# Performance work log

Hardware: AMD Instinct MI355X
Metric: run time of the kernel (lower is better)

## Reference

```python
import jax, jax.numpy as jnp
import numpy as np

B, N, D0 = 128, 128, 512   # batch, n_objects, obj_dim
H, KD, R = 32, 64, 16      # n_heads, key_dim, n_relations
D = D0 + 1                 # with temporal tag

def setup_inputs() -> dict:
    key = jax.random.key(0)
    k1, k2, k3, k4, k5 = jax.random.split(key, 5)
    s = 0.02
    return {
        'obj_seq': jax.random.normal(k1, (B, N, D0), jnp.float32),
        'W_k':  jax.random.normal(k2, (KD, D), jnp.float32) * s,
        'W_q1': jax.random.normal(k3, (H * KD, D * N), jnp.float32) * s,
        'W_q2': jax.random.normal(k4, (H * KD, D * N), jnp.float32) * s,
        'W_s':  jax.random.normal(k5, (R, D), jnp.float32) * s,
    }

def reference(obj_seq, W_k, W_q1, W_q2, W_s):
    b, n, _ = obj_seq.shape
    # append temporal tag channel: obj -> [B, N, D]
    tag = jnp.broadcast_to(jnp.arange(n, dtype=obj_seq.dtype)[None, :, None], (b, n, 1))
    obj = jnp.concatenate([obj_seq, tag], axis=2)
    flat = obj.reshape(b, -1)                      # [B, N*D]
    Q1 = (flat @ W_q1.T).reshape(b, H, KD)         # [B, H, KD]
    Q2 = (flat @ W_q2.T).reshape(b, H, KD)
    K = obj @ W_k.T                                # [B, N, KD]
    # scores [B, N, H], softmax over objects (dim=1 in torch)
    A1 = jax.nn.softmax(jnp.einsum('bhk,bnk->bnh', Q1, K), axis=1)
    A2 = jax.nn.softmax(jnp.einsum('bhk,bnk->bnh', Q2, K), axis=1)
    # attention-weighted object sums: [B, H, D]
    E1 = jnp.einsum('bnh,bnd->bhd', A1, obj)
    E2 = jnp.einsum('bnh,bnd->bhd', A2, obj)
    Dr = E1 @ W_s.T - E2 @ W_s.T                   # [B, H, R]
    Dr = jnp.concatenate([Dr, E1[:, :, -1:], E2[:, :, -1:]], axis=2)  # [B, H, R+2]
    return Dr.reshape(b, -1)                       # [B, H*(R+2)]
```

## Files before the change

### kernel.cpp

```cpp
#include <hip/hip_runtime.h>
#include <cstdint>

typedef _Float16 f16;
typedef _Float16 f16x8 __attribute__((ext_vector_type(8)));
typedef short s16x8 __attribute__((ext_vector_type(8)));
typedef unsigned u32x4 __attribute__((ext_vector_type(4)));
typedef float f32x4 __attribute__((ext_vector_type(4)));
typedef float floatx4 __attribute__((ext_vector_type(4)));

#define KTOT 65664
#define KSTEPS 2052
#define DP 544

__device__ __forceinline__ void gload_lds16(const void* g, void* l) {
  __builtin_amdgcn_global_load_lds(
      (const __attribute__((address_space(1))) void*)g,
      (__attribute__((address_space(3))) void*)l, 16, 0, 0);
}

__device__ __forceinline__ unsigned bfpack(float e0, float e1) {
  return (__float_as_uint(e0) >> 16) | (__float_as_uint(e1) & 0xffff0000u);
}
__device__ __forceinline__ float bfhi(float x) {
  return __uint_as_float(__float_as_uint(x) & 0xffff0000u);
}

__global__ void prep_flat(const float* __restrict__ obj_seq, char* __restrict__ flatA) {
  int o = blockIdx.x * 256 + threadIdx.x;
  int row = o & 127;
  int k8 = (o >> 7) & 3;
  int pl = (o >> 9) & 1;
  int kb = o >> 10;
  int k0 = kb * 32 + k8 * 8;
  unsigned w[4];
#pragma unroll
  for (int j = 0; j < 8; j += 2) {
    float v[2];
#pragma unroll
    for (int jj = 0; jj < 2; ++jj) {
      int k = k0 + j + jj;
      int n = k / 513;
      int d = k - n * 513;
      float x = (d < 512) ? obj_seq[(((size_t)(row << 7) + n) << 9) + d] : (float)n;
      if (pl) x = x - bfhi(x);
      v[jj] = x;
    }
    w[j >> 1] = bfpack(v[0], v[1]);
  }
  *(u32x4*)(flatA + (size_t)o * 16) = (u32x4){w[0], w[1], w[2], w[3]};
}

__global__ void prep_obj(const float* __restrict__ obj_seq, f16* __restrict__ objHi,
                         f16* __restrict__ objLo, f16* __restrict__ objT16) {
  __shared__ f16 tile[32][132];
  int b = blockIdx.x / 17, c = blockIdx.x - 17 * (blockIdx.x / 17);
  int t = threadIdx.x;
  if (c < 16) {
#pragma unroll
    for (int i = 0; i < 16; ++i) {
      int e = t + i * 256;
      int n = e >> 5, dd = e & 31;
      float v = obj_seq[(((size_t)(b << 7) + n) << 9) + (c << 5) + dd];
      f16 h = (f16)v;
      objHi[((size_t)((b << 7) + n)) * DP + (c << 5) + dd] = h;
      objLo[((size_t)((b << 7) + n)) * DP + (c << 5) + dd] = (f16)(v - (float)h);
      tile[dd][n] = h;
    }
    __syncthreads();
#pragma unroll
    for (int i = 0; i < 16; ++i) {
      int e = t + i * 256;
      int dd = e >> 7, n = e & 127;
      objT16[(((size_t)b * DP + (c << 5) + dd) << 7) + n] = tile[dd][n];
    }
  } else {
#pragma unroll
    for (int i = 0; i < 16; ++i) {
      int e = t + i * 256;
      int n = e >> 5, dd = e & 31;
      f16 h = (dd == 0) ? (f16)(float)n : (f16)0.f;
      objHi[((size_t)((b << 7) + n)) * DP + 512 + dd] = h;
      objLo[((size_t)((b << 7) + n)) * DP + 512 + dd] = (f16)0.f;
    }
#pragma unroll
    for (int i = 0; i < 16; ++i) {
      int e = t + i * 256;
      int dd = e >> 7, n = e & 127;
      objT16[(((size_t)b * DP + 512 + dd) << 7) + n] = (dd == 0) ? (f16)(float)n : (f16)0.f;
    }
  }
}

__global__ void prep_wk(const float* __restrict__ W_k, f16* __restrict__ WkHi,
                        f16* __restrict__ WkLo) {
  int o = blockIdx.x * 256 + threadIdx.x;
  int kd = o / DP, d = o - kd * DP;
  float v = (d < 513) ? W_k[kd * 513 + d] * 1024.f : 0.f;
  f16 h = (f16)v;
  WkHi[o] = h;
  WkLo[o] = (f16)(v - (float)h);
}

__global__ __launch_bounds__(512, 4) void qgemm(const char* __restrict__ flatA,
                                                const float* __restrict__ Wq1,
                                                const float* __restrict__ Wq2,
                                                float* __restrict__ Qpart) {
  __shared__ __align__(16) char smem[65536];
  const int tid = threadIdx.x;
  const int lane = tid & 63;
  const int wave = tid >> 6;
  const int wm = wave >> 2, wn = wave & 3;
  const int l15 = lane & 15, lk = lane >> 4;
  const int ntile = blockIdx.x & 31;
  const int ksp = blockIdx.x >> 5;
  const int t0 = ksp * 129;
  const int nt = min(129, KSTEPS - t0);
  const float* Wsrc = (ntile < 16) ? (Wq1 + (size_t)ntile * 128 * KTOT)
                                   : (Wq2 + (size_t)(ntile - 16) * 128 * KTOT);

  const char* asrc = flatA + (size_t)t0 * 16384 + tid * 16;
  const float* wsrc0;
  const float* wsrc1;
  {
    int c0 = (tid >> 3), c1 = 64 + (tid >> 3);
    wsrc0 = Wsrc + (size_t)c0 * KTOT + (size_t)t0 * 32 + (((tid & 7) ^ (c0 & 7)) << 2);
    wsrc1 = Wsrc + (size_t)c1 * KTOT + (size_t)t0 * 32 + (((tid & 7) ^ (c1 & 7)) << 2);
  }

  int aoff[2][4];
#pragma unroll
  for (int pl = 0; pl < 2; ++pl)
#pragma unroll
    for (int mi = 0; mi < 4; ++mi)
      aoff[pl][mi] = pl * 8192 + lk * 2048 + (wm * 64 + mi * 16 + l15) * 16;
  int woff[2][2];
#pragma unroll
  for (int nf = 0; nf < 2; ++nf) {
    int col = wn * 32 + nf * 16 + l15;
#pragma unroll
    for (int j = 0; j < 2; ++j)
      woff[nf][j] = 16384 + col * 128 + (((2 * lk + j) ^ (col & 7)) << 4);
  }

  f32x4 acc[4][2];
#pragma unroll
  for (int mi = 0; mi < 4; ++mi)
#pragma unroll
    for (int nf = 0; nf < 2; ++nf) acc[mi][nf] = (f32x4){0.f, 0.f, 0.f, 0.f};

  auto stage = [&](int tt) {
    char* S = smem + (tt & 1) * 32768;
    gload_lds16(asrc + (size_t)tt * 16384, S + tid * 16);
    gload_lds16(asrc + (size_t)tt * 16384 + 8192, S + 8192 + tid * 16);
    gload_lds16(wsrc0 + (size_t)tt * 32, S + 16384 + tid * 16);
    gload_lds16(wsrc1 + (size_t)tt * 32, S + 24576 + tid * 16);
  };

  auto compute = [&](const char* S) {
    s16x8 wH[2], wL[2];
#pragma unroll
    for (int nf = 0; nf < 2; ++nf) {
      floatx4 a = *(const floatx4*)(S + woff[nf][0]);
      floatx4 b = *(const floatx4*)(S + woff[nf][1]);
      u32x4 H = (u32x4){bfpack(a[0], a[1]), bfpack(a[2], a[3]),
                        bfpack(b[0], b[1]), bfpack(b[2], b[3])};
      float l0 = a[0] - bfhi(a[0]), l1 = a[1] - bfhi(a[1]);
      float l2 = a[2] - bfhi(a[2]), l3 = a[3] - bfhi(a[3]);
      float l4 = b[0] - bfhi(b[0]), l5 = b[1] - bfhi(b[1]);
      float l6 = b[2] - bfhi(b[2]), l7 = b[3] - bfhi(b[3]);
      u32x4 L = (u32x4){bfpack(l0, l1), bfpack(l2, l3), bfpack(l4, l5), bfpack(l6, l7)};
      wH[nf] = *(s16x8*)&H;
      wL[nf] = *(s16x8*)&L;
    }
#pragma unroll
    for (int mi = 0; mi < 4; ++mi) {
      s16x8 aH = *(const s16x8*)(S + aoff[0][mi]);
      s16x8 aL = *(const s16x8*)(S + aoff[1][mi]);
#pragma unroll
      for (int nf = 0; nf < 2; ++nf) {
        acc[mi][nf] = __builtin_amdgcn_mfma_f32_16x16x32_bf16(aH, wH[nf], acc[mi][nf], 0, 0, 0);
        acc[mi][nf] = __builtin_amdgcn_mfma_f32_16x16x32_bf16(aH, wL[nf], acc[mi][nf], 0, 0, 0);
        acc[mi][nf] = __builtin_amdgcn_mfma_f32_16x16x32_bf16(aL, wH[nf], acc[mi][nf], 0, 0, 0);
      }
    }
  };

  stage(0);
  stage(1);

  for (int t = 0; t < nt; ++t) {
    if (t < nt - 1) asm volatile("s_waitcnt vmcnt(4)" ::: "memory");
    else            asm volatile("s_waitcnt vmcnt(0)" ::: "memory");
    __builtin_amdgcn_s_barrier();
    __builtin_amdgcn_sched_barrier(0);
    compute(smem + (t & 1) * 32768);
    __builtin_amdgcn_sched_barrier(0);
    __builtin_amdgcn_s_barrier();
    if (t + 2 < nt) stage(t + 2);
  }

  float* qout = Qpart + (size_t)ksp * 524288;
#pragma unroll
  for (int mi = 0; mi < 4; ++mi) {
    int row = wm * 64 + mi * 16 + lk * 4;
#pragma unroll
    for (int nf = 0; nf < 2; ++nf) {
      int col = ntile * 128 + wn * 32 + nf * 16 + l15;
#pragma unroll
      for (int j = 0; j < 4; ++j)
        qout[(size_t)(row + j) * 4096 + col] = acc[mi][nf][j];
    }
  }
}

__global__ __launch_bounds__(512, 1) void predinet_tail(
    const f16* __restrict__ objHi, const f16* __restrict__ objLo, const f16* __restrict__ objT16,
    const f16* __restrict__ WkHi, const f16* __restrict__ WkLo,
    const float* __restrict__ Qpart, const float* __restrict__ W_s, float* __restrict__ out) {
  __shared__ __align__(16) char smem[105984];
  const int b = blockIdx.x;
  const int tid = threadIdx.x, lane = tid & 63, wave = tid >> 6;
  const int l15 = lane & 15, lk = lane >> 4;

  f16* WT = (f16*)(smem);
  f16* Qh = (f16*)(smem + 17408);
  f16* Ql = (f16*)(smem + 26624);
  f16* Kh = (f16*)(smem + 35840);
  f16* Kl = (f16*)(smem + 54272);
  float* S = (float*)(smem + 72704);
  f16* E = (f16*)(smem + 17408);
  float* DL = (float*)(smem + 96832);

  {
    const float* qp = Qpart + (size_t)b * 4096 + tid * 8;
    floatx4 q0 = (floatx4){0.f, 0.f, 0.f, 0.f};
    floatx4 q1 = (floatx4){0.f, 0.f, 0.f, 0.f};
#pragma unroll
    for (int p = 0; p < 16; ++p) {
      q0 += *(const floatx4*)(qp + (size_t)p * 524288);
      q1 += *(const floatx4*)(qp + (size_t)p * 524288 + 4);
    }
    int hp = tid >> 3, kd = (tid * 8) & 63;
    f16x8 vh, vl;
#pragma unroll
    for (int j = 0; j < 4; ++j) {
      f16 h0 = (f16)q0[j]; vh[j] = h0; vl[j] = (f16)(q0[j] - (float)h0);
      f16 h1 = (f16)q1[j]; vh[4 + j] = h1; vl[4 + j] = (f16)(q1[j] - (float)h1);
    }
    *(f16x8*)(Qh + hp * 72 + kd) = vh;
    *(f16x8*)(Ql + hp * 72 + kd) = vl;
  }
  {
    f32x4 acc[4];
#pragma unroll
    for (int nf = 0; nf < 4; ++nf) acc[nf] = (f32x4){0.f, 0.f, 0.f, 0.f};
    const f16* arowH = objHi + ((size_t)(b * 128) + wave * 16 + l15) * DP + lk * 8;
    const f16* arowL = objLo + ((size_t)(b * 128) + wave * 16 + l15) * DP + lk * 8;
    const f16* bhi = WkHi + (size_t)l15 * DP + lk * 8;
    const f16* blo = WkLo + (size_t)l15 * DP + lk * 8;
    for (int ks = 0; ks < 17; ++ks) {
      f16x8 ah = *(const f16x8*)(arowH + ks * 32);
      f16x8 al = *(const f16x8*)(arowL + ks * 32);
#pragma unroll
      for (int nf = 0; nf < 4; ++nf) {
        f16x8 h = *(const f16x8*)(bhi + (size_t)nf * 16 * DP + ks * 32);
        f16x8 l = *(const f16x8*)(blo + (size_t)nf * 16 * DP + ks * 32);
        acc[nf] = __builtin_amdgcn_mfma_f32_16x16x32_f16(ah, h, acc[nf], 0, 0, 0);
        acc[nf] = __builtin_amdgcn_mfma_f32_16x16x32_f16(ah, l, acc[nf], 0, 0, 0);
        acc[nf] = __builtin_amdgcn_mfma_f32_16x16x32_f16(al, h, acc[nf], 0, 0, 0);
      }
    }
#pragma unroll
    for (int nf = 0; nf < 4; ++nf)
#pragma unroll
      for (int j = 0; j < 4; ++j) {
        float kv = acc[nf][j] * (1.f / 1024.f);
        f16 h = (f16)kv;
        Kh[(wave * 16 + lk * 4 + j) * 72 + nf * 16 + l15] = h;
        Kl[(wave * 16 + lk * 4 + j) * 72 + nf * 16 + l15] = (f16)(kv - (float)h);
      }
  }
  __syncthreads();
  {
    f32x4 acc[4];
#pragma unroll
    for (int nf = 0; nf < 4; ++nf) acc[nf] = (f32x4){0.f, 0.f, 0.f, 0.f};
#pragma unroll
    for (int ks = 0; ks < 2; ++ks) {
      f16x8 ah = *(const f16x8*)(Kh + (wave * 16 + l15) * 72 + ks * 32 + lk * 8);
      f16x8 al = *(const f16x8*)(Kl + (wave * 16 + l15) * 72 + ks * 32 + lk * 8);
#pragma unroll
      for (int nf = 0; nf < 4; ++nf) {
        f16x8 bh = *(const f16x8*)(Qh + (nf * 16 + l15) * 72 + ks * 32 + lk * 8);
        f16x8 bl = *(const f16x8*)(Ql + (nf * 16 + l15) * 72 + ks * 32 + lk * 8);
        acc[nf] = __builtin_amdgcn_mfma_f32_16x16x32_f16(ah, bh, acc[nf], 0, 0, 0);
        acc[nf] = __builtin_amdgcn_mfma_f32_16x16x32_f16(ah, bl, acc[nf], 0, 0, 0);
        acc[nf] = __builtin_amdgcn_mfma_f32_16x16x32_f16(al, bh, acc[nf], 0, 0, 0);
      }
    }
#pragma unroll
    for (int nf = 0; nf < 4; ++nf)
#pragma unroll
      for (int j = 0; j < 4; ++j)
        S[(wave * 16 + lk * 4 + j) * 65 + nf * 16 + l15] = acc[nf][j];
  }
  __syncthreads();
  {
#pragma unroll
    for (int ci = 0; ci < 8; ++ci) {
      int c = wave * 8 + ci;
      float s0 = S[lane * 65 + c], s1 = S[(lane + 64) * 65 + c];
      float m = fmaxf(s0, s1);
      for (int off = 32; off; off >>= 1) m = fmaxf(m, __shfl_xor(m, off));
      float e0 = __expf(s0 - m), e1 = __expf(s1 - m);
      float sum = e0 + e1;
      for (int off = 32; off; off >>= 1) sum += __shfl_xor(sum, off);
      float inv = 1.f / sum;
      WT[c * 136 + lane] = (f16)(e0 * inv);
      WT[c * 136 + 64 + lane] = (f16)(e1 * inv);
    }
  }
  __syncthreads();
  {
    f16x8 bw[4][4];
#pragma unroll
    for (int nf = 0; nf < 4; ++nf)
#pragma unroll
      for (int ks = 0; ks < 4; ++ks)
        bw[nf][ks] = *(const f16x8*)(WT + (nf * 16 + l15) * 136 + ks * 32 + lk * 8);
    for (int r = 0; r < 5; ++r) {
      int mi = r * 8 + wave;
      if (mi >= 34) break;
      const f16* arow = objT16 + (((size_t)b * DP + mi * 16 + l15) << 7) + lk * 8;
      f16x8 a[4];
#pragma unroll
      for (int ks = 0; ks < 4; ++ks) a[ks] = *(const f16x8*)(arow + ks * 32);
#pragma unroll
      for (int nf = 0; nf < 4; ++nf) {
        f32x4 acc = (f32x4){0.f, 0.f, 0.f, 0.f};
#pragma unroll
        for (int ks = 0; ks < 4; ++ks)
          acc = __builtin_amdgcn_mfma_f32_16x16x32_f16(a[ks], bw[nf][ks], acc, 0, 0, 0);
#pragma unroll
        for (int j = 0; j < 4; ++j)
          E[(mi * 16 + lk * 4 + j) * 73 + nf * 16 + l15] = (f16)acc[j];
      }
    }
  }
  __syncthreads();
  {
    f16* Ws16 = WT;
    for (int i = tid; i < 16 * DP; i += 512) {
      int r = i / DP, d = i - r * DP;
      Ws16[i] = (f16)((d < 513) ? W_s[r * 513 + d] : 0.f);
    }
  }
  __syncthreads();
  if (wave < 4) {
    const f16* Ws16 = WT;
    f32x4 acc = (f32x4){0.f, 0.f, 0.f, 0.f};
    for (int ks = 0; ks < 17; ++ks) {
      f16x8 a = *(const f16x8*)(Ws16 + l15 * DP + ks * 32 + lk * 8);
      f16x8 bv;
#pragma unroll
      for (int jj = 0; jj < 8; ++jj)
        bv[jj] = E[(ks * 32 + lk * 8 + jj) * 73 + wave * 16 + l15];
      acc = __builtin_amdgcn_mfma_f32_16x16x32_f16(a, bv, acc, 0, 0, 0);
    }
#pragma unroll
    for (int j = 0; j < 4; ++j) DL[(lk * 4 + j) * 64 + wave * 16 + l15] = acc[j];
  }
  __syncthreads();
  {
    int h = tid >> 4, r = tid & 15;
    float v = DL[r * 64 + h] - DL[r * 64 + 32 + h];
    out[(size_t)b * 576 + h * 18 + r] = v;
    if (tid < 64) {
      int set = tid >> 5, hh = tid & 31;
      out[(size_t)b * 576 + hh * 18 + 16 + set] = (float)E[512 * 73 + set * 32 + hh];
    }
  }
}

extern "C" void kernel_launch(void* const* d_in, const int* in_sizes, int n_in,
                              void* d_out, int out_size, void* d_ws, size_t ws_size,
                              hipStream_t stream) {
  const float* obj_seq = (const float*)d_in[0];
  const float* W_k = (const float*)d_in[1];
  const float* W_q1 = (const float*)d_in[2];
  const float* W_q2 = (const float*)d_in[3];
  const float* W_s = (const float*)d_in[4];
  float* out = (float*)d_out;

  char* ws = (char*)d_ws;
  size_t off = 0;
  auto carve = [&](size_t bytes) -> char* {
    char* p = ws + off;
    off += (bytes + 255) & ~(size_t)255;
    return p;
  };
  char* flatA = carve((size_t)KSTEPS * 16384);
  f16* objHi = (f16*)carve((size_t)16384 * DP * 2);
  f16* objLo = (f16*)carve((size_t)16384 * DP * 2);
  f16* objT16 = (f16*)carve((size_t)128 * DP * 128 * 2);
  f16* WkHi = (f16*)carve((size_t)64 * DP * 2);
  f16* WkLo = (f16*)carve((size_t)64 * DP * 2);
  float* Qpart = (float*)carve((size_t)16 * 524288 * 4);
  (void)ws_size; (void)in_sizes; (void)n_in; (void)out_size;

  prep_flat<<<8208, 256, 0, stream>>>(obj_seq, flatA);
  prep_obj<<<2176, 256, 0, stream>>>(obj_seq, objHi, objLo, objT16);
  prep_wk<<<136, 256, 0, stream>>>(W_k, WkHi, WkLo);
  qgemm<<<512, 512, 0, stream>>>(flatA, W_q1, W_q2, Qpart);
  predinet_tail<<<128, 512, 0, stream>>>(objHi, objLo, objT16, WkHi, WkLo, Qpart, W_s, out);
}
```

Baseline: 366.8 us.

## Widen Q-GEMM tile to 256 columns with triple-buffered LDS pipeline

Each qgemm block now covers 256 output columns instead of 128, so the launch drops to 256 blocks and each fp32 flat activation tile is re-read from global memory half as often. Weight and activation stages are split into three LDS slots, which removes the second barrier per iteration. Weight loads for step t+2 are issued before the compute and activation loads after it. MFMA sections are wrapped in s_setprio, and the larger 144KB LDS footprint means only one block fits per CU, which lowers occupancy and latency hiding.

```diff
diff --git a/kernel.cpp b/kernel.cpp
--- a/kernel.cpp
+++ b/kernel.cpp
@@ -101,30 +101,30 @@
   WkLo[o] = (f16)(v - (float)h);
 }
 
-__global__ __launch_bounds__(512, 4) void qgemm(const char* __restrict__ flatA,
+__global__ __launch_bounds__(512, 2) void qgemm(const char* __restrict__ flatA,
                                                 const float* __restrict__ Wq1,
                                                 const float* __restrict__ Wq2,
                                                 float* __restrict__ Qpart) {
-  __shared__ __align__(16) char smem[65536];
+  __shared__ __align__(16) char smem[147456];
   const int tid = threadIdx.x;
   const int lane = tid & 63;
   const int wave = tid >> 6;
   const int wm = wave >> 2, wn = wave & 3;
   const int l15 = lane & 15, lk = lane >> 4;
-  const int ntile = blockIdx.x & 31;
-  const int ksp = blockIdx.x >> 5;
+  const int ntile = blockIdx.x & 15;
+  const int ksp = blockIdx.x >> 4;
   const int t0 = ksp * 129;
   const int nt = min(129, KSTEPS - t0);
-  const float* Wsrc = (ntile < 16) ? (Wq1 + (size_t)ntile * 128 * KTOT)
-                                   : (Wq2 + (size_t)(ntile - 16) * 128 * KTOT);
+  const float* Wsrc = (ntile < 8) ? (Wq1 + (size_t)ntile * 256 * KTOT)
+                                  : (Wq2 + (size_t)(ntile - 8) * 256 * KTOT);
 
   const char* asrc = flatA + (size_t)t0 * 16384 + tid * 16;
-  const float* wsrc0;
-  const float* wsrc1;
-  {
-    int c0 = (tid >> 3), c1 = 64 + (tid >> 3);
-    wsrc0 = Wsrc + (size_t)c0 * KTOT + (size_t)t0 * 32 + (((tid & 7) ^ (c0 & 7)) << 2);
-    wsrc1 = Wsrc + (size_t)c1 * KTOT + (size_t)t0 * 32 + (((tid & 7) ^ (c1 & 7)) << 2);
+  const float* wsrcs[4];
+#pragma unroll
+  for (int c = 0; c < 4; ++c) {
+    int col = c * 64 + (tid >> 3);
+    int gs = (tid & 7) ^ (col & 7);
+    wsrcs[c] = Wsrc + (size_t)col * KTOT + (size_t)t0 * 32 + gs * 4;
   }
 
   int aoff[2][4];
@@ -133,35 +133,39 @@
 #pragma unroll
     for (int mi = 0; mi < 4; ++mi)
       aoff[pl][mi] = pl * 8192 + lk * 2048 + (wm * 64 + mi * 16 + l15) * 16;
-  int woff[2][2];
-#pragma unroll
-  for (int nf = 0; nf < 2; ++nf) {
-    int col = wn * 32 + nf * 16 + l15;
+  int woff[4][2];
+#pragma unroll
+  for (int nf = 0; nf < 4; ++nf) {
+    int col = wn * 64 + nf * 16 + l15;
 #pragma unroll
     for (int j = 0; j < 2; ++j)
-      woff[nf][j] = 16384 + col * 128 + (((2 * lk + j) ^ (col & 7)) << 4);
-  }
-
-  f32x4 acc[4][2];
+      woff[nf][j] = col * 128 + (((2 * lk + j) ^ (col & 7)) << 4);
+  }
+
+  f32x4 acc[4][4];
 #pragma unroll
   for (int mi = 0; mi < 4; ++mi)
 #pragma unroll
-    for (int nf = 0; nf < 2; ++nf) acc[mi][nf] = (f32x4){0.f, 0.f, 0.f, 0.f};
-
-  auto stage = [&](int tt) {
-    char* S = smem + (tt & 1) * 32768;
+    for (int nf = 0; nf < 4; ++nf) acc[mi][nf] = (f32x4){0.f, 0.f, 0.f, 0.f};
+
+  auto stageW = [&](int tt, int slot) {
+    char* S = smem + 49152 + slot * 32768;
+#pragma unroll
+    for (int c = 0; c < 4; ++c)
+      gload_lds16(wsrcs[c] + (size_t)tt * 32, S + c * 8192 + tid * 16);
+  };
+  auto stageA = [&](int tt, int slot) {
+    char* S = smem + slot * 16384;
     gload_lds16(asrc + (size_t)tt * 16384, S + tid * 16);
     gload_lds16(asrc + (size_t)tt * 16384 + 8192, S + 8192 + tid * 16);
-    gload_lds16(wsrc0 + (size_t)tt * 32, S + 16384 + tid * 16);
-    gload_lds16(wsrc1 + (size_t)tt * 32, S + 24576 + tid * 16);
   };
 
-  auto compute = [&](const char* S) {
-    s16x8 wH[2], wL[2];
-#pragma unroll
-    for (int nf = 0; nf < 2; ++nf) {
-      floatx4 a = *(const floatx4*)(S + woff[nf][0]);
-      floatx4 b = *(const floatx4*)(S + woff[nf][1]);
+  auto compute = [&](const char* SA, const char* SW) {
+    s16x8 wH[4], wL[4];
+#pragma unroll
+    for (int nf = 0; nf < 4; ++nf) {
+      floatx4 a = *(const floatx4*)(SW + woff[nf][0]);
+      floatx4 b = *(const floatx4*)(SW + woff[nf][1]);
       u32x4 H = (u32x4){bfpack(a[0], a[1]), bfpack(a[2], a[3]),
                         bfpack(b[0], b[1]), bfpack(b[2], b[3])};
       float l0 = a[0] - bfhi(a[0]), l1 = a[1] - bfhi(a[1]);
@@ -172,31 +176,36 @@
       wH[nf] = *(s16x8*)&H;
       wL[nf] = *(s16x8*)&L;
     }
+    __builtin_amdgcn_s_setprio(1);
 #pragma unroll
     for (int mi = 0; mi < 4; ++mi) {
-      s16x8 aH = *(const s16x8*)(S + aoff[0][mi]);
-      s16x8 aL = *(const s16x8*)(S + aoff[1][mi]);
-#pragma unroll
-      for (int nf = 0; nf < 2; ++nf) {
+      s16x8 aH = *(const s16x8*)(SA + aoff[0][mi]);
+      s16x8 aL = *(const s16x8*)(SA + aoff[1][mi]);
+#pragma unroll
+      for (int nf = 0; nf < 4; ++nf) {
         acc[mi][nf] = __builtin_amdgcn_mfma_f32_16x16x32_bf16(aH, wH[nf], acc[mi][nf], 0, 0, 0);
         acc[mi][nf] = __builtin_amdgcn_mfma_f32_16x16x32_bf16(aH, wL[nf], acc[mi][nf], 0, 0, 0);
         acc[mi][nf] = __builtin_amdgcn_mfma_f32_16x16x32_bf16(aL, wH[nf], acc[mi][nf], 0, 0, 0);
       }
     }
+    __builtin_amdgcn_s_setprio(0);
   };
 
-  stage(0);
-  stage(1);
-
+  stageW(0, 0); stageA(0, 0);
+  stageW(1, 1); stageA(1, 1);
+
+  int sl = 0;
   for (int t = 0; t < nt; ++t) {
-    if (t < nt - 1) asm volatile("s_waitcnt vmcnt(4)" ::: "memory");
+    if (t < nt - 2) asm volatile("s_waitcnt vmcnt(6)" ::: "memory");
     else            asm volatile("s_waitcnt vmcnt(0)" ::: "memory");
     __builtin_amdgcn_s_barrier();
     __builtin_amdgcn_sched_barrier(0);
-    compute(smem + (t & 1) * 32768);
+    int s2 = sl + 2; if (s2 >= 3) s2 -= 3;
+    if (t + 2 < nt) stageW(t + 2, s2);
     __builtin_amdgcn_sched_barrier(0);
-    __builtin_amdgcn_s_barrier();
-    if (t + 2 < nt) stage(t + 2);
+    compute(smem + sl * 16384, smem + 49152 + sl * 32768);
+    if (t + 2 < nt) stageA(t + 2, s2);
+    sl = (sl == 2) ? 0 : sl + 1;
   }
 
   float* qout = Qpart + (size_t)ksp * 524288;
@@ -204,8 +213,8 @@
   for (int mi = 0; mi < 4; ++mi) {
     int row = wm * 64 + mi * 16 + lk * 4;
 #pragma unroll
-    for (int nf = 0; nf < 2; ++nf) {
-      int col = ntile * 128 + wn * 32 + nf * 16 + l15;
+    for (int nf = 0; nf < 4; ++nf) {
+      int col = ntile * 256 + wn * 64 + nf * 16 + l15;
 #pragma unroll
       for (int j = 0; j < 4; ++j)
         qout[(size_t)(row + j) * 4096 + col] = acc[mi][nf][j];
@@ -411,6 +420,6 @@
   prep_flat<<<8208, 256, 0, stream>>>(obj_seq, flatA);
   prep_obj<<<2176, 256, 0, stream>>>(obj_seq, objHi, objLo, objT16);
   prep_wk<<<136, 256, 0, stream>>>(W_k, WkHi, WkLo);
-  qgemm<<<512, 512, 0, stream>>>(flatA, W_q1, W_q2, Qpart);
+  qgemm<<<256, 512, 0, stream>>>(flatA, W_q1, W_q2, Qpart);
   predinet_tail<<<128, 512, 0, stream>>>(objHi, objLo, objT16, WkHi, WkLo, Qpart, W_s, out);
 }
```

Result: faster. 350.9 us (median of 2 runs) (-4.3%).

## Deepen qgemm prefetch pipeline with separate A/W ring buffers and halve split-K

Applied to the files above, without the earlier changes.

Splits the qgemm LDS staging into a 3-slot ring for activations and a 7-slot ring for the fp32 weights, so weight loads are issued up to six steps ahead. Only one barrier remains per k-step, and MFMA sections run at raised wave priority. The split-K factor drops from 16 to 8, so 256 workgroups each own 160KB of LDS and the tail sums fewer partials. This is meant to keep more weight traffic in flight in a bandwidth-bound GEMM. In exchange, occupancy falls to one block per CU, and the last iterations issue redundant clamped loads.

```diff
diff --git a/kernel.cpp b/kernel.cpp
--- a/kernel.cpp
+++ b/kernel.cpp
@@ -101,11 +101,11 @@
   WkLo[o] = (f16)(v - (float)h);
 }
 
-__global__ __launch_bounds__(512, 4) void qgemm(const char* __restrict__ flatA,
+__global__ __launch_bounds__(512, 2) void qgemm(const char* __restrict__ flatA,
                                                 const float* __restrict__ Wq1,
                                                 const float* __restrict__ Wq2,
                                                 float* __restrict__ Qpart) {
-  __shared__ __align__(16) char smem[65536];
+  __shared__ __align__(16) char smem[163840];
   const int tid = threadIdx.x;
   const int lane = tid & 63;
   const int wave = tid >> 6;
@@ -113,8 +113,8 @@
   const int l15 = lane & 15, lk = lane >> 4;
   const int ntile = blockIdx.x & 31;
   const int ksp = blockIdx.x >> 5;
-  const int t0 = ksp * 129;
-  const int nt = min(129, KSTEPS - t0);
+  const int t0 = (KSTEPS * ksp) >> 3;
+  const int nt = ((KSTEPS * (ksp + 1)) >> 3) - t0;
   const float* Wsrc = (ntile < 16) ? (Wq1 + (size_t)ntile * 128 * KTOT)
                                    : (Wq2 + (size_t)(ntile - 16) * 128 * KTOT);
 
@@ -139,7 +139,7 @@
     int col = wn * 32 + nf * 16 + l15;
 #pragma unroll
     for (int j = 0; j < 2; ++j)
-      woff[nf][j] = 16384 + col * 128 + (((2 * lk + j) ^ (col & 7)) << 4);
+      woff[nf][j] = col * 128 + (((2 * lk + j) ^ (col & 7)) << 4);
   }
 
   f32x4 acc[4][2];
@@ -148,34 +148,38 @@
 #pragma unroll
     for (int nf = 0; nf < 2; ++nf) acc[mi][nf] = (f32x4){0.f, 0.f, 0.f, 0.f};
 
-  auto stage = [&](int tt) {
-    char* S = smem + (tt & 1) * 32768;
+  auto stageA = [&](int tt, int slot) {
+    char* S = smem + slot * 16384;
     gload_lds16(asrc + (size_t)tt * 16384, S + tid * 16);
     gload_lds16(asrc + (size_t)tt * 16384 + 8192, S + 8192 + tid * 16);
-    gload_lds16(wsrc0 + (size_t)tt * 32, S + 16384 + tid * 16);
-    gload_lds16(wsrc1 + (size_t)tt * 32, S + 24576 + tid * 16);
   };
-
-  auto compute = [&](const char* S) {
+  auto stageW = [&](int tt, int slot) {
+    char* S = smem + 49152 + slot * 16384;
+    gload_lds16(wsrc0 + (size_t)tt * 32, S + tid * 16);
+    gload_lds16(wsrc1 + (size_t)tt * 32, S + 8192 + tid * 16);
+  };
+
+  auto compute = [&](const char* SA, const char* SW) {
     s16x8 wH[2], wL[2];
 #pragma unroll
     for (int nf = 0; nf < 2; ++nf) {
-      floatx4 a = *(const floatx4*)(S + woff[nf][0]);
-      floatx4 b = *(const floatx4*)(S + woff[nf][1]);
+      floatx4 a = *(const floatx4*)(SW + woff[nf][0]);
+      floatx4 b = *(const floatx4*)(SW + woff[nf][1]);
       u32x4 H = (u32x4){bfpack(a[0], a[1]), bfpack(a[2], a[3]),
                         bfpack(b[0], b[1]), bfpack(b[2], b[3])};
       float l0 = a[0] - bfhi(a[0]), l1 = a[1] - bfhi(a[1]);
       float l2 = a[2] - bfhi(a[2]), l3 = a[3] - bfhi(a[3]);
       float l4 = b[0] - bfhi(b[0]), l5 = b[1] - bfhi(b[1]);
-      float l6 = b[2] - bfhi(b[2]), l7 = b[3] - bfhi(b[3]);
+      float l6 = b[2] - bfhi(b[2]), l7 = b[3] - bfhi(b[7 - 7 + 3]);
       u32x4 L = (u32x4){bfpack(l0, l1), bfpack(l2, l3), bfpack(l4, l5), bfpack(l6, l7)};
       wH[nf] = *(s16x8*)&H;
       wL[nf] = *(s16x8*)&L;
     }
+    __builtin_amdgcn_s_setprio(1);
 #pragma unroll
     for (int mi = 0; mi < 4; ++mi) {
-      s16x8 aH = *(const s16x8*)(S + aoff[0][mi]);
-      s16x8 aL = *(const s16x8*)(S + aoff[1][mi]);
+      s16x8 aH = *(const s16x8*)(SA + aoff[0][mi]);
+      s16x8 aL = *(const s16x8*)(SA + aoff[1][mi]);
 #pragma unroll
       for (int nf = 0; nf < 2; ++nf) {
         acc[mi][nf] = __builtin_amdgcn_mfma_f32_16x16x32_bf16(aH, wH[nf], acc[mi][nf], 0, 0, 0);
@@ -183,21 +187,34 @@
         acc[mi][nf] = __builtin_amdgcn_mfma_f32_16x16x32_bf16(aL, wH[nf], acc[mi][nf], 0, 0, 0);
       }
     }
+    __builtin_amdgcn_s_setprio(0);
   };
 
-  stage(0);
-  stage(1);
-
+  stageW(0, 0); stageW(1, 1); stageW(2, 2); stageW(3, 3);
+  stageA(0, 0);
+  stageW(4, 4);
+  stageA(1, 1);
+  stageW(5, 5);
+
+  int sa = 0, sw = 0, sa2 = 2, sw6 = 6;
   for (int t = 0; t < nt; ++t) {
-    if (t < nt - 1) asm volatile("s_waitcnt vmcnt(4)" ::: "memory");
-    else            asm volatile("s_waitcnt vmcnt(0)" ::: "memory");
+    asm volatile("s_waitcnt vmcnt(6)" ::: "memory");
     __builtin_amdgcn_s_barrier();
     __builtin_amdgcn_sched_barrier(0);
-    compute(smem + (t & 1) * 32768);
+    {
+      int ta = t + 2; if (ta > nt - 1) ta = nt - 1;
+      int tw = t + 6; if (tw > nt - 1) tw = nt - 1;
+      stageA(ta, sa2);
+      stageW(tw, sw6);
+    }
     __builtin_amdgcn_sched_barrier(0);
-    __builtin_amdgcn_s_barrier();
-    if (t + 2 < nt) stage(t + 2);
-  }
+    compute(smem + sa * 16384, smem + 49152 + sw * 16384);
+    sa = (sa == 2) ? 0 : sa + 1;
+    sa2 = (sa2 == 2) ? 0 : sa2 + 1;
+    sw = (sw == 6) ? 0 : sw + 1;
+    sw6 = (sw6 == 6) ? 0 : sw6 + 1;
+  }
+  asm volatile("s_waitcnt vmcnt(0)" ::: "memory");
 
   float* qout = Qpart + (size_t)ksp * 524288;
 #pragma unroll
@@ -236,7 +253,7 @@
     floatx4 q0 = (floatx4){0.f, 0.f, 0.f, 0.f};
     floatx4 q1 = (floatx4){0.f, 0.f, 0.f, 0.f};
 #pragma unroll
-    for (int p = 0; p < 16; ++p) {
+    for (int p = 0; p < 8; ++p) {
       q0 += *(const floatx4*)(qp + (size_t)p * 524288);
       q1 += *(const floatx4*)(qp + (size_t)p * 524288 + 4);
     }
@@ -405,12 +422,12 @@
   f16* objT16 = (f16*)carve((size_t)128 * DP * 128 * 2);
   f16* WkHi = (f16*)carve((size_t)64 * DP * 2);
   f16* WkLo = (f16*)carve((size_t)64 * DP * 2);
-  float* Qpart = (float*)carve((size_t)16 * 524288 * 4);
+  float* Qpart = (float*)carve((size_t)8 * 524288 * 4);
   (void)ws_size; (void)in_sizes; (void)n_in; (void)out_size;
 
   prep_flat<<<8208, 256, 0, stream>>>(obj_seq, flatA);
   prep_obj<<<2176, 256, 0, stream>>>(obj_seq, objHi, objLo, objT16);
   prep_wk<<<136, 256, 0, stream>>>(W_k, WkHi, WkLo);
-  qgemm<<<512, 512, 0, stream>>>(flatA, W_q1, W_q2, Qpart);
+  qgemm<<<256, 512, 0, stream>>>(flatA, W_q1, W_q2, Qpart);
   predinet_tail<<<128, 512, 0, stream>>>(objHi, objLo, objT16, WkHi, WkLo, Qpart, W_s, out);
 }
```

New measurement: 367.7 us. No clear change (+0.2%).
